# Performance work log

Measured on AMD Instinct MI355X. Metric: run time of the kernel, lower is better.

Reference implementation:

```python
import jax, jax.numpy as jnp
import numpy as np

B, N, DIM = 1, 100_000, 512
HEADS, DIM_HEAD, M = 8, 64, 64


def setup_inputs() -> dict:
    key = jax.random.key(0)
    ks = jax.random.split(key, 9)
    s = 0.04  # ~ kaiming-ish scale for dim=512
    return {
        "x": jax.random.normal(ks[0], (B, N, DIM), dtype=jnp.float32),
        "temperature": jnp.full((1, HEADS, 1, 1), 0.5, dtype=jnp.float32),
        "w_slice": jax.random.normal(ks[1], (HEADS * M, DIM), dtype=jnp.float32) * s,
        "b_slice": jnp.zeros((HEADS * M,), dtype=jnp.float32),
        "w1": jax.random.normal(ks[2], (DIM_HEAD, DIM), dtype=jnp.float32) * s,
        "b1": jnp.zeros((DIM_HEAD,), dtype=jnp.float32),
        "wq": jax.random.normal(ks[3], (DIM_HEAD, DIM_HEAD), dtype=jnp.float32) * 0.125,
        "wk": jax.random.normal(ks[4], (DIM_HEAD, DIM_HEAD), dtype=jnp.float32) * 0.125,
        "wv": jax.random.normal(ks[5], (DIM_HEAD, DIM_HEAD), dtype=jnp.float32) * 0.125,
        "w3": jax.random.normal(ks[6], (DIM_HEAD, DIM_HEAD), dtype=jnp.float32) * 0.125,
        "b3": jnp.zeros((DIM_HEAD,), dtype=jnp.float32),
    }


def reference(x, temperature, w_slice, b_slice, w1, b1, wq, wk, wv, w3, b3):
    b, n, c = x.shape
    # slice logits: (B,N,H*M) -> (B,H,N,M)
    logits = jnp.einsum("bnc,ec->bne", x, w_slice) + b_slice
    logits = logits.reshape(b, n, HEADS, M).transpose(0, 2, 1, 3)
    temp = jnp.clip(temperature, 0.1, 5.0)
    w = jax.nn.softmax(logits / temp, axis=-1)          # (B,H,N,M)
    d = w.sum(axis=2)                                    # (B,H,M)
    # N -> M aggregation (w^T @ x per head)
    s_raw = jnp.einsum("bhnm,bnc->bhmc", w, x)          # (B,H,M,C)
    s = jnp.einsum("bhmc,dc->bhmd", s_raw / (d[..., None] + 1e-5), w1) + b1  # (B,H,M,dh)
    q = jnp.einsum("bhmd,ed->bhme", s, wq)
    k = jnp.einsum("bhmd,ed->bhme", s, wk)
    v = jnp.einsum("bhmd,ed->bhme", s, wv)
    scale = 1.0 / jnp.sqrt(jnp.asarray(DIM_HEAD, dtype=s.dtype))
    attn = jax.nn.softmax(jnp.einsum("bhme,bhle->bhml", q, k) * scale, axis=-1)
    s_att = jnp.einsum("bhml,bhle->bhme", attn, v)      # (B,H,M,dh)
    s_out = jnp.einsum("bhme,de->bhmd", s_att, w3) + b3
    # deslice: w @ s_out -> (B,H,N,dh) -> (B,N,H*dh)
    x_out = jnp.einsum("bhnm,bhmd->bhnd", w, s_out)
    return x_out.transpose(0, 2, 1, 3).reshape(b, n, HEADS * DIM_HEAD)
```

## Files before the change

kernel.cpp:

```cpp
#include <hip/hip_runtime.h>

typedef _Float16 f16;
typedef _Float16 f16x8 __attribute__((ext_vector_type(8)));
typedef _Float16 f16x4 __attribute__((ext_vector_type(4)));
typedef float    f32x4 __attribute__((ext_vector_type(4)));

#define N_TOK   100000
#define NPAD    100032
#define NT1     1563
#define CDIM    512
#define KSTEPS  (NPAD/32)
#define K2SPL   128

#define O_WT     ((size_t)0)
#define SZ_WT    ((size_t)512*NPAD*2)
#define O_YT     (O_WT + SZ_WT)
#define SZ_YT    ((size_t)64*NPAD*2)
#define O_WFR    (O_YT + SZ_YT)
#define SZ_WFR   ((size_t)16*4*9*64*8*2)
#define O_SPP    (O_WFR + SZ_WFR)
#define SZ_SPP   ((size_t)K2SPL*32768*4)
#define O_DPP    (O_SPP + SZ_SPP)
#define SZ_DPP   ((size_t)K2SPL*512*4)
#define O_SPRE   (O_DPP + SZ_DPP)
#define SZ_SPRE  ((size_t)32768*4)
#define O_DSTD   (O_SPRE + SZ_SPRE)
#define SZ_DSTD  ((size_t)512*4)
#define O_SOUT   (O_DSTD + SZ_DSTD)
#define SZ_SOUT  ((size_t)8*64*64*2)

__global__ void k0_pack(const float* __restrict__ wsf, const float* __restrict__ w1f,
                        f16* __restrict__ wfr) {
    int c = blockIdx.x * 256 + threadIdx.x;
    int lane = c & 63, g = c >> 6;
    int u  = g % 9,  r = g / 9;
    int we = r & 3,  kg = r >> 2;
    int col = lane & 15, quad = lane >> 4;
    int k = kg * 32 + quad * 8;
    const float* src;
    if (u < 8) src = wsf + (size_t)(we*128 + u*16 + col) * CDIM + k;
    else       src = w1f + (size_t)(we*16  + col) * CDIM + k;
    float4 a = *(const float4*)(src);
    float4 b = *(const float4*)(src + 4);
    f16x8 h;
    h[0]=(f16)a.x; h[1]=(f16)a.y; h[2]=(f16)a.z; h[3]=(f16)a.w;
    h[4]=(f16)b.x; h[5]=(f16)b.y; h[6]=(f16)b.z; h[7]=(f16)b.w;
    *(f16x8*)(wfr + (size_t)c * 8) = h;
}

#define XROW 40
#define TPITCH 72
__launch_bounds__(256, 3)
__global__ void k1_slice(const float* __restrict__ x, const float* __restrict__ temperature,
                         const f16* __restrict__ wfr, const float* __restrict__ bsl,
                         f16* __restrict__ wT, f16* __restrict__ yT) {
    __shared__ f16 smem[256 * TPITCH];
    f16* lX = smem;
    f16* lT = smem;

    const int tid  = threadIdx.x;
    const int wave = tid >> 6;
    const int lane = tid & 63;
    const int quad = lane >> 4;
    const int col  = lane & 15;

    const int b = blockIdx.x;
    int nt, hg;
    if (b < 3120) { nt = (b >> 4) * 8 + (b & 7); hg = (b >> 3) & 1; }
    else          { nt = 1560 + ((b - 3120) >> 1); hg = (b - 3120) & 1; }
    const int hgrp = hg;
    const int n0   = nt * 64;
    const int h    = hgrp * 4 + wave;

    const int srow = tid >> 2, sch = tid & 3;
    int snr = n0 + srow; if (snr > N_TOK - 1) snr = N_TOK - 1;
    const float* sbase = x + (size_t)snr * CDIM + sch * 8;

    {
        float4 a = *(const float4*)(sbase);
        float4 bb = *(const float4*)(sbase + 4);
        f16x8 hh;
        hh[0]=(f16)a.x; hh[1]=(f16)a.y; hh[2]=(f16)a.z; hh[3]=(f16)a.w;
        hh[4]=(f16)bb.x; hh[5]=(f16)bb.y; hh[6]=(f16)bb.z; hh[7]=(f16)bb.w;
        *(f16x8*)(&lX[srow * XROW + sch * 8]) = hh;
    }

    f32x4 acc[4][5];
    #pragma unroll
    for (int nf = 0; nf < 4; ++nf)
        #pragma unroll
        for (int u = 0; u < 5; ++u) acc[nf][u] = f32x4{0.f,0.f,0.f,0.f};

    __syncthreads();

    #pragma unroll 2
    for (int kg = 0; kg < 16; ++kg) {
        const f16* wb = wfr + ((size_t)(kg*4 + (h >> 1)) * 9 + (size_t)(h & 1) * 4) * 512
                            + (size_t)lane * 8;
        f16x8 bf[4];
        #pragma unroll
        for (int j = 0; j < 4; ++j) bf[j] = *(const f16x8*)(wb + j * 512);
        f16x8 bfy;
        if (hgrp == 0)
            bfy = *(const f16x8*)(wfr + ((size_t)(kg*4 + wave) * 9 + 8) * 512 + (size_t)lane * 8);

        float4 xa, xb;
        if (kg < 15) {
            xa = *(const float4*)(sbase + (kg + 1) * 32);
            xb = *(const float4*)(sbase + (kg + 1) * 32 + 4);
        }

        const f16* xbuf = lX + (kg & 1) * (64 * XROW);
        f16x8 af[4];
        #pragma unroll
        for (int nf = 0; nf < 4; ++nf)
            af[nf] = *(const f16x8*)(xbuf + (nf*16 + col) * XROW + quad * 8);

        #pragma unroll
        for (int nf = 0; nf < 4; ++nf)
            #pragma unroll
            for (int j = 0; j < 4; ++j)
                acc[nf][j] = __builtin_amdgcn_mfma_f32_16x16x32_f16(af[nf], bf[j], acc[nf][j], 0, 0, 0);
        if (hgrp == 0) {
            #pragma unroll
            for (int nf = 0; nf < 4; ++nf)
                acc[nf][4] = __builtin_amdgcn_mfma_f32_16x16x32_f16(af[nf], bfy, acc[nf][4], 0, 0, 0);
        }

        if (kg < 15) {
            f16x8 hh;
            hh[0]=(f16)xa.x; hh[1]=(f16)xa.y; hh[2]=(f16)xa.z; hh[3]=(f16)xa.w;
            hh[4]=(f16)xb.x; hh[5]=(f16)xb.y; hh[6]=(f16)xb.z; hh[7]=(f16)xb.w;
            *(f16x8*)(&lX[((kg + 1) & 1) * (64 * XROW) + srow * XROW + sch * 8]) = hh;
        }
        __syncthreads();
    }

    #pragma unroll
    for (int j = 0; j < 4; ++j) {
        float bb = bsl[h*64 + j*16 + col];
        #pragma unroll
        for (int nf = 0; nf < 4; ++nf)
            #pragma unroll
            for (int r = 0; r < 4; ++r) acc[nf][j][r] += bb;
    }
    float tv = temperature[h];
    tv = fminf(fmaxf(tv, 0.1f), 5.0f);
    const float invt = 1.0f / tv;

    #pragma unroll
    for (int nf = 0; nf < 4; ++nf) {
        const int nloc = nf*16 + quad*4;
        float mx[4];
        #pragma unroll
        for (int r = 0; r < 4; ++r) {
            float m01 = fmaxf(acc[nf][0][r], acc[nf][1][r]);
            float m23 = fmaxf(acc[nf][2][r], acc[nf][3][r]);
            mx[r] = fmaxf(m01, m23);
        }
        #pragma unroll
        for (int d = 1; d < 16; d <<= 1)
            #pragma unroll
            for (int r = 0; r < 4; ++r) mx[r] = fmaxf(mx[r], __shfl_xor(mx[r], d));
        float sm[4] = {0.f, 0.f, 0.f, 0.f};
        #pragma unroll
        for (int j = 0; j < 4; ++j)
            #pragma unroll
            for (int r = 0; r < 4; ++r) {
                float ev = __expf((acc[nf][j][r] - mx[r]) * invt);
                acc[nf][j][r] = ev;
                sm[r] += ev;
            }
        #pragma unroll
        for (int d = 1; d < 16; d <<= 1)
            #pragma unroll
            for (int r = 0; r < 4; ++r) sm[r] += __shfl_xor(sm[r], d);
        #pragma unroll
        for (int r = 0; r < 4; ++r) sm[r] = 1.0f / sm[r];
        #pragma unroll
        for (int j = 0; j < 4; ++j) {
            f16x4 pk;
            #pragma unroll
            for (int r = 0; r < 4; ++r) {
                int n = n0 + nloc + r;
                float wv = (n < N_TOK) ? acc[nf][j][r] * sm[r] : 0.0f;
                pk[r] = (f16)wv;
            }
            int e_loc = wave*64 + j*16 + col;
            *(f16x4*)(lT + (size_t)e_loc*TPITCH + nloc) = pk;
        }
        if (hgrp == 0) {
            f16x4 pk;
            #pragma unroll
            for (int r = 0; r < 4; ++r) {
                int n = n0 + nloc + r;
                pk[r] = (n < N_TOK) ? (f16)acc[nf][4][r] : (f16)0.f;
            }
            *(f16x4*)(yT + (size_t)(wave*16 + col) * NPAD + n0 + nloc) = pk;
        }
    }
    __syncthreads();

    #pragma unroll
    for (int i = 0; i < 8; ++i) {
        int id = tid + i*256;
        int e = id >> 3, p = id & 7;
        f16x8 v = *(const f16x8*)(lT + (size_t)e*TPITCH + p*8);
        *(f16x8*)(wT + (size_t)(hgrp*256 + e)*NPAD + n0 + p*8) = v;
    }
}

#define K2_LOAD(AF, BF, kss)                                                         \
    {   int nb_ = (kss)*32 + quad*8;                                                 \
        _Pragma("unroll")                                                            \
        for (int v = 0; v < 4; ++v)                                                  \
            BF[v] = *(const f16x8*)(yT + (size_t)(v*16 + col)*NPAD + nb_);           \
        _Pragma("unroll")                                                            \
        for (int u = 0; u < 2; ++u)                                                  \
            AF[u] = *(const f16x8*)(wT + (size_t)(ebase + u*16 + col)*NPAD + nb_);   \
    }
#define K2_MFMA(AF, BF)                                                              \
    {   _Pragma("unroll")                                                            \
        for (int u = 0; u < 2; ++u) {                                                \
            _Pragma("unroll")                                                        \
            for (int v = 0; v < 4; ++v)                                              \
                acc[u][v] = __builtin_amdgcn_mfma_f32_16x16x32_f16(AF[u], BF[v], acc[u][v], 0, 0, 0); \
            float s_ = 0.f;                                                          \
            _Pragma("unroll")                                                        \
            for (int j = 0; j < 8; ++j) s_ += (float)AF[u][j];                       \
            dac[u] += s_;                                                            \
        }                                                                            \
    }
__launch_bounds__(256, 4)
__global__ void k2_spre(const f16* __restrict__ wT, const f16* __restrict__ yT,
                        float* __restrict__ spp, float* __restrict__ dpp) {
    const int tid = threadIdx.x, wave = tid >> 6, lane = tid & 63;
    const int quad = lane >> 4, col = lane & 15;
    const int slot = blockIdx.x >> 2, equad = blockIdx.x & 3;
    const int ebase = equad * 128 + wave * 32;

    const int ks0 = (slot * KSTEPS) >> 7;
    const int ks1 = ((slot + 1) * KSTEPS) >> 7;

    f32x4 acc[2][4];
    float dac[2];
    #pragma unroll
    for (int u = 0; u < 2; ++u) {
        dac[u] = 0.f;
        #pragma unroll
        for (int v = 0; v < 4; ++v) acc[u][v] = f32x4{0.f,0.f,0.f,0.f};
    }

    f16x8 afA[2], bfA[4], afB[2], bfB[4];
    K2_LOAD(afA, bfA, ks0)
    int ks = ks0;
    for (; ks + 2 <= ks1; ks += 2) {
        K2_LOAD(afB, bfB, ks + 1)
        K2_MFMA(afA, bfA)
        K2_LOAD(afA, bfA, ks + 2)
        K2_MFMA(afB, bfB)
    }
    if (ks < ks1) K2_MFMA(afA, bfA)

    #pragma unroll
    for (int u = 0; u < 2; ++u) {
        dac[u] += __shfl_xor(dac[u], 16);
        dac[u] += __shfl_xor(dac[u], 32);
    }
    if (quad == 0) {
        #pragma unroll
        for (int u = 0; u < 2; ++u)
            dpp[slot*512 + ebase + u*16 + col] = dac[u];
    }
    float* dst = spp + (size_t)slot * 32768 + (size_t)equad * 8192;
    #pragma unroll
    for (int u = 0; u < 2; ++u)
        #pragma unroll
        for (int v = 0; v < 4; ++v)
            *(f32x4*)(dst + (size_t)((wave*2 + u)*4 + v)*256 + (size_t)lane*4) = acc[u][v];
}

__global__ void k2r_reduce(const float* __restrict__ spp, const float* __restrict__ dpp,
                           float* __restrict__ spre, float* __restrict__ dstd) {
    int i = blockIdx.x*256 + threadIdx.x;
    float s = 0.f;
    for (int p = 0; p < K2SPL; ++p) s += spp[(size_t)p*32768 + i];
    int r = i & 3, L = (i >> 2) & 63, v = (i >> 8) & 3, g = (i >> 10) & 7, eq = (i >> 13) & 3;
    int e = eq*128 + (g >> 1)*32 + (g & 1)*16 + (L >> 4)*4 + r;
    int d = v*16 + (L & 15);
    spre[e*64 + d] = s;
    if (i < 512) {
        float tt = 0.f;
        for (int p = 0; p < K2SPL; ++p) tt += dpp[p*512 + i];
        dstd[i] = tt;
    }
}

__global__ void k3_attn(const float* __restrict__ spre, const float* __restrict__ dstd,
                        const float* __restrict__ b1, const float* __restrict__ wq,
                        const float* __restrict__ wk, const float* __restrict__ wv,
                        const float* __restrict__ w3, const float* __restrict__ b3,
                        f16* __restrict__ sout) {
    __shared__ float wa[64][65], wb[64][65], wc[64][65];
    __shared__ float ss[64][65], kk[64][65], vv[64][65];
    __shared__ float qq[16][65], sc[16][65];
    const int h = blockIdx.x >> 2, ms = blockIdx.x & 3, tid = threadIdx.x;

    for (int i = tid; i < 4096; i += 256) {
        int r = i >> 6, c = i & 63;
        wa[r][c] = wq[i];
        wb[r][c] = wk[i];
        wc[r][c] = wv[i];
        ss[r][c] = spre[h*4096 + i] / (dstd[h*64 + r] + 1e-5f) + b1[c];
    }
    __syncthreads();

    #pragma unroll
    for (int it = 0; it < 16; ++it) {
        int m = it*4 + (tid >> 6), e = tid & 63;
        float ak = 0.f, av = 0.f;
        #pragma unroll 8
        for (int d = 0; d < 64; ++d) {
            float sv = ss[m][d];
            ak += sv * wb[e][d];
            av += sv * wc[e][d];
        }
        kk[m][e] = ak; vv[m][e] = av;
    }
    #pragma unroll
    for (int it = 0; it < 4; ++it) {
        int ml = it*4 + (tid >> 6), e = tid & 63;
        float aq = 0.f;
        #pragma unroll 8
        for (int d = 0; d < 64; ++d) aq += ss[ms*16 + ml][d] * wa[e][d];
        qq[ml][e] = aq;
    }
    __syncthreads();

    for (int i = tid; i < 4096; i += 256) wa[i >> 6][i & 63] = w3[i];
    #pragma unroll
    for (int it = 0; it < 4; ++it) {
        int ml = it*4 + (tid >> 6), l = tid & 63;
        float a = 0.f;
        #pragma unroll 8
        for (int e = 0; e < 64; ++e) a += qq[ml][e] * kk[l][e];
        sc[ml][l] = a * 0.125f;
    }
    __syncthreads();

    if (tid < 16) {
        int ml = tid;
        float mx = -1e30f;
        #pragma unroll 8
        for (int l = 0; l < 64; ++l) mx = fmaxf(mx, sc[ml][l]);
        float sm = 0.f;
        #pragma unroll 8
        for (int l = 0; l < 64; ++l) { float ev = __expf(sc[ml][l] - mx); sc[ml][l] = ev; sm += ev; }
        float rs = 1.0f / sm;
        #pragma unroll 8
        for (int l = 0; l < 64; ++l) sc[ml][l] *= rs;
    }
    __syncthreads();

    #pragma unroll
    for (int it = 0; it < 4; ++it) {
        int ml = it*4 + (tid >> 6), e = tid & 63;
        float a = 0.f;
        #pragma unroll 8
        for (int l = 0; l < 64; ++l) a += sc[ml][l] * vv[l][e];
        qq[ml][e] = a;
    }
    __syncthreads();

    #pragma unroll
    for (int it = 0; it < 4; ++it) {
        int d = it*16 + (tid >> 4), ml = tid & 15;
        float a = b3[d];
        #pragma unroll 8
        for (int e = 0; e < 64; ++e) a += qq[ml][e] * wa[d][e];
        sout[(h*64 + d)*64 + ms*16 + ml] = (f16)a;
    }
}

#define K4PITCH 36
__launch_bounds__(256, 4)
__global__ void k4_deslice(const f16* __restrict__ wT, const f16* __restrict__ sout,
                           float* __restrict__ out) {
    __shared__ __align__(16) char lmem[512 * K4PITCH * 2];
    f16*   ldsW = (f16*)lmem;
    float* ldsO = (float*)lmem;

    const int tid = threadIdx.x, wave = tid >> 6, lane = tid & 63;
    const int quad = lane >> 4, col = lane & 15;

    const int bid = blockIdx.x;
    const int xcd = bid & 7, idx = bid >> 3;
    const int q = KSTEPS >> 3, r = KSTEPS & 7;
    const int swz = (xcd < r ? xcd*(q+1) : r*(q+1) + (xcd - r)*q) + idx;
    const int n0 = swz * 32;

    #pragma unroll
    for (int i = 0; i < 8; ++i) {
        int id = tid + i*256;
        int e = id >> 2, p = id & 3;
        f16x8 v = *(const f16x8*)(wT + (size_t)e*NPAD + n0 + p*8);
        *(f16x8*)(ldsW + (size_t)e*K4PITCH + p*8) = v;
    }
    __syncthreads();

    f32x4 acc[2][2][4];
    #pragma unroll
    for (int hh = 0; hh < 2; ++hh)
        #pragma unroll
        for (int t = 0; t < 2; ++t)
            #pragma unroll
            for (int v = 0; v < 4; ++v) acc[hh][t][v] = f32x4{0.f,0.f,0.f,0.f};

    #pragma unroll
    for (int hh = 0; hh < 2; ++hh) {
        int h = wave*2 + hh;
        #pragma unroll
        for (int ks = 0; ks < 2; ++ks) {
            f16x8 af[2], bf[4];
            #pragma unroll
            for (int t = 0; t < 2; ++t) {
                f16x8 a;
                #pragma unroll
                for (int j = 0; j < 8; ++j)
                    a[j] = ldsW[(size_t)(h*64 + ks*32 + quad*8 + j)*K4PITCH + t*16 + col];
                af[t] = a;
            }
            #pragma unroll
            for (int v = 0; v < 4; ++v)
                bf[v] = *(const f16x8*)(sout + (size_t)(h*64 + v*16 + col)*64 + ks*32 + quad*8);
            #pragma unroll
            for (int t = 0; t < 2; ++t)
                #pragma unroll
                for (int v = 0; v < 4; ++v)
                    acc[hh][t][v] = __builtin_amdgcn_mfma_f32_16x16x32_f16(af[t], bf[v], acc[hh][t][v], 0, 0, 0);
        }
    }

    #pragma unroll
    for (int p = 0; p < 2; ++p) {
        __syncthreads();
        #pragma unroll
        for (int hh = 0; hh < 2; ++hh) {
            int h = wave*2 + hh;
            #pragma unroll
            for (int v = 0; v < 4; ++v)
                #pragma unroll
                for (int r2 = 0; r2 < 4; ++r2)
                    ldsO[(size_t)(quad*4 + r2)*516 + h*64 + v*16 + col] = acc[hh][p][v][r2];
        }
        __syncthreads();
        #pragma unroll
        for (int it = 0; it < 8; ++it) {
            int id = tid + it*256;
            int row = id >> 7, ch = id & 127;
            int n = n0 + p*16 + row;
            if (n < N_TOK) {
                float4 v4 = *(const float4*)(ldsO + (size_t)row*516 + ch*4);
                *(float4*)(out + (size_t)n*512 + ch*4) = v4;
            }
        }
    }
}

extern "C" void kernel_launch(void* const* d_in, const int* in_sizes, int n_in,
                              void* d_out, int out_size, void* d_ws, size_t ws_size,
                              hipStream_t stream) {
    const float* x           = (const float*)d_in[0];
    const float* temperature = (const float*)d_in[1];
    const float* w_slice     = (const float*)d_in[2];
    const float* b_slice     = (const float*)d_in[3];
    const float* w1          = (const float*)d_in[4];
    const float* b1          = (const float*)d_in[5];
    const float* wq          = (const float*)d_in[6];
    const float* wk          = (const float*)d_in[7];
    const float* wv          = (const float*)d_in[8];
    const float* w3          = (const float*)d_in[9];
    const float* b3          = (const float*)d_in[10];
    float* out = (float*)d_out;
    char*  ws  = (char*)d_ws;

    f16*   wT    = (f16*)(ws + O_WT);
    f16*   yT    = (f16*)(ws + O_YT);
    f16*   wfr   = (f16*)(ws + O_WFR);
    float* spp   = (float*)(ws + O_SPP);
    float* dpp   = (float*)(ws + O_DPP);
    float* spre  = (float*)(ws + O_SPRE);
    float* dstd  = (float*)(ws + O_DSTD);
    f16*   sout  = (f16*)(ws + O_SOUT);

    k0_pack<<<144, 256, 0, stream>>>(w_slice, w1, wfr);
    k1_slice<<<NT1*2, 256, 0, stream>>>(x, temperature, wfr, b_slice, wT, yT);
    k2_spre<<<K2SPL*4, 256, 0, stream>>>(wT, yT, spp, dpp);
    k2r_reduce<<<128, 256, 0, stream>>>(spp, dpp, spre, dstd);
    k3_attn<<<32, 256, 0, stream>>>(spre, dstd, b1, wq, wk, wv, w3, b3, sout);
    k4_deslice<<<KSTEPS, 256, 0, stream>>>(wT, sout, out);
}
```

Before: 563.0 us.

## Split slice kernel work across more blocks with 2 heads per block

```diff
diff --git a/kernel.cpp b/kernel.cpp
--- a/kernel.cpp
+++ b/kernel.cpp
@@ -50,27 +50,27 @@
 
 #define XROW 40
 #define TPITCH 72
-__launch_bounds__(256, 3)
+__launch_bounds__(256, 4)
 __global__ void k1_slice(const float* __restrict__ x, const float* __restrict__ temperature,
                          const f16* __restrict__ wfr, const float* __restrict__ bsl,
                          f16* __restrict__ wT, f16* __restrict__ yT) {
-    __shared__ f16 smem[256 * TPITCH];
+    __shared__ f16 smem[128 * TPITCH];
     f16* lX = smem;
     f16* lT = smem;
 
     const int tid  = threadIdx.x;
-    const int wave = tid >> 6;
+    const int w    = tid >> 6;
     const int lane = tid & 63;
     const int quad = lane >> 4;
     const int col  = lane & 15;
 
     const int b = blockIdx.x;
     int nt, hg;
-    if (b < 3120) { nt = (b >> 4) * 8 + (b & 7); hg = (b >> 3) & 1; }
-    else          { nt = 1560 + ((b - 3120) >> 1); hg = (b - 3120) & 1; }
-    const int hgrp = hg;
-    const int n0   = nt * 64;
-    const int h    = hgrp * 4 + wave;
+    if (b < 6240) { nt = (b >> 5) * 8 + (b & 7); hg = (b >> 3) & 3; }
+    else          { int t = b - 6240; nt = 1560 + (t >> 2); hg = t & 3; }
+    const int n0 = nt * 64;
+    const int hd = hg * 2 + (w & 1);
+    const int nh = w >> 1;
 
     const int srow = tid >> 2, sch = tid & 3;
     int snr = n0 + srow; if (snr > N_TOK - 1) snr = N_TOK - 1;
@@ -85,24 +85,32 @@
         *(f16x8*)(&lX[srow * XROW + sch * 8]) = hh;
     }
 
-    f32x4 acc[4][5];
-    #pragma unroll
-    for (int nf = 0; nf < 4; ++nf)
-        #pragma unroll
-        for (int u = 0; u < 5; ++u) acc[nf][u] = f32x4{0.f,0.f,0.f,0.f};
+    f32x4 accS[2][4];
+    f32x4 accY[2][2];
+    #pragma unroll
+    for (int nf = 0; nf < 2; ++nf) {
+        #pragma unroll
+        for (int j = 0; j < 4; ++j) accS[nf][j] = f32x4{0.f,0.f,0.f,0.f};
+        #pragma unroll
+        for (int jy = 0; jy < 2; ++jy) accY[nf][jy] = f32x4{0.f,0.f,0.f,0.f};
+    }
 
     __syncthreads();
 
     #pragma unroll 2
     for (int kg = 0; kg < 16; ++kg) {
-        const f16* wb = wfr + ((size_t)(kg*4 + (h >> 1)) * 9 + (size_t)(h & 1) * 4) * 512
+        const f16* wb = wfr + ((size_t)(kg*4 + (hd >> 1)) * 9 + (size_t)(hd & 1) * 4) * 512
                             + (size_t)lane * 8;
         f16x8 bf[4];
         #pragma unroll
         for (int j = 0; j < 4; ++j) bf[j] = *(const f16x8*)(wb + j * 512);
-        f16x8 bfy;
-        if (hgrp == 0)
-            bfy = *(const f16x8*)(wfr + ((size_t)(kg*4 + wave) * 9 + 8) * 512 + (size_t)lane * 8);
+        f16x8 bfy[2];
+        if (hg == 0) {
+            #pragma unroll
+            for (int jy = 0; jy < 2; ++jy)
+                bfy[jy] = *(const f16x8*)(wfr + ((size_t)(kg*4 + ((w & 1)*2 + jy)) * 9 + 8) * 512
+                                               + (size_t)lane * 8);
+        }
 
         float4 xa, xb;
         if (kg < 15) {
@@ -111,20 +119,22 @@
         }
 
         const f16* xbuf = lX + (kg & 1) * (64 * XROW);
-        f16x8 af[4];
-        #pragma unroll
-        for (int nf = 0; nf < 4; ++nf)
-            af[nf] = *(const f16x8*)(xbuf + (nf*16 + col) * XROW + quad * 8);
-
-        #pragma unroll
-        for (int nf = 0; nf < 4; ++nf)
+        f16x8 af[2];
+        #pragma unroll
+        for (int nf = 0; nf < 2; ++nf)
+            af[nf] = *(const f16x8*)(xbuf + (nh*32 + nf*16 + col) * XROW + quad * 8);
+
+        #pragma unroll
+        for (int nf = 0; nf < 2; ++nf)
             #pragma unroll
             for (int j = 0; j < 4; ++j)
-                acc[nf][j] = __builtin_amdgcn_mfma_f32_16x16x32_f16(af[nf], bf[j], acc[nf][j], 0, 0, 0);
-        if (hgrp == 0) {
-            #pragma unroll
-            for (int nf = 0; nf < 4; ++nf)
-                acc[nf][4] = __builtin_amdgcn_mfma_f32_16x16x32_f16(af[nf], bfy, acc[nf][4], 0, 0, 0);
+                accS[nf][j] = __builtin_amdgcn_mfma_f32_16x16x32_f16(af[nf], bf[j], accS[nf][j], 0, 0, 0);
+        if (hg == 0) {
+            #pragma unroll
+            for (int nf = 0; nf < 2; ++nf)
+                #pragma unroll
+                for (int jy = 0; jy < 2; ++jy)
+                    accY[nf][jy] = __builtin_amdgcn_mfma_f32_16x16x32_f16(af[nf], bfy[jy], accY[nf][jy], 0, 0, 0);
         }
 
         if (kg < 15) {
@@ -138,24 +148,24 @@
 
     #pragma unroll
     for (int j = 0; j < 4; ++j) {
-        float bb = bsl[h*64 + j*16 + col];
-        #pragma unroll
-        for (int nf = 0; nf < 4; ++nf)
-            #pragma unroll
-            for (int r = 0; r < 4; ++r) acc[nf][j][r] += bb;
-    }
-    float tv = temperature[h];
+        float bb = bsl[hd*64 + j*16 + col];
+        #pragma unroll
+        for (int nf = 0; nf < 2; ++nf)
+            #pragma unroll
+            for (int r = 0; r < 4; ++r) accS[nf][j][r] += bb;
+    }
+    float tv = temperature[hd];
     tv = fminf(fmaxf(tv, 0.1f), 5.0f);
     const float invt = 1.0f / tv;
 
     #pragma unroll
-    for (int nf = 0; nf < 4; ++nf) {
-        const int nloc = nf*16 + quad*4;
+    for (int nf = 0; nf < 2; ++nf) {
+        const int nloc = nh*32 + nf*16 + quad*4;
         float mx[4];
         #pragma unroll
         for (int r = 0; r < 4; ++r) {
-            float m01 = fmaxf(acc[nf][0][r], acc[nf][1][r]);
-            float m23 = fmaxf(acc[nf][2][r], acc[nf][3][r]);
+            float m01 = fmaxf(accS[nf][0][r], accS[nf][1][r]);
+            float m23 = fmaxf(accS[nf][2][r], accS[nf][3][r]);
             mx[r] = fmaxf(m01, m23);
         }
         #pragma unroll
@@ -167,8 +177,8 @@
         for (int j = 0; j < 4; ++j)
             #pragma unroll
             for (int r = 0; r < 4; ++r) {
-                float ev = __expf((acc[nf][j][r] - mx[r]) * invt);
-                acc[nf][j][r] = ev;
+                float ev = __expf((accS[nf][j][r] - mx[r]) * invt);
+                accS[nf][j][r] = ev;
                 sm[r] += ev;
             }
         #pragma unroll
@@ -183,30 +193,34 @@
             #pragma unroll
             for (int r = 0; r < 4; ++r) {
                 int n = n0 + nloc + r;
-                float wv = (n < N_TOK) ? acc[nf][j][r] * sm[r] : 0.0f;
+                float wv = (n < N_TOK) ? accS[nf][j][r] * sm[r] : 0.0f;
                 pk[r] = (f16)wv;
             }
-            int e_loc = wave*64 + j*16 + col;
+            int e_loc = (w & 1)*64 + j*16 + col;
             *(f16x4*)(lT + (size_t)e_loc*TPITCH + nloc) = pk;
         }
-        if (hgrp == 0) {
-            f16x4 pk;
-            #pragma unroll
-            for (int r = 0; r < 4; ++r) {
-                int n = n0 + nloc + r;
-                pk[r] = (n < N_TOK) ? (f16)acc[nf][4][r] : (f16)0.f;
+        if (hg == 0) {
+            #pragma unroll
+            for (int jy = 0; jy < 2; ++jy) {
+                f16x4 pk;
+                #pragma unroll
+                for (int r = 0; r < 4; ++r) {
+                    int n = n0 + nloc + r;
+                    pk[r] = (n < N_TOK) ? (f16)accY[nf][jy][r] : (f16)0.f;
+                }
+                int d = ((w & 1)*2 + jy)*16 + col;
+                *(f16x4*)(yT + (size_t)d * NPAD + n0 + nloc) = pk;
             }
-            *(f16x4*)(yT + (size_t)(wave*16 + col) * NPAD + n0 + nloc) = pk;
-        }
-    }
-    __syncthreads();
-
-    #pragma unroll
-    for (int i = 0; i < 8; ++i) {
+        }
+    }
+    __syncthreads();
+
+    #pragma unroll
+    for (int i = 0; i < 4; ++i) {
         int id = tid + i*256;
         int e = id >> 3, p = id & 7;
         f16x8 v = *(const f16x8*)(lT + (size_t)e*TPITCH + p*8);
-        *(f16x8*)(wT + (size_t)(hgrp*256 + e)*NPAD + n0 + p*8) = v;
+        *(f16x8*)(wT + (size_t)(hg*128 + e)*NPAD + n0 + p*8) = v;
     }
 }
 
@@ -303,8 +317,8 @@
                         f16* __restrict__ sout) {
     __shared__ float wa[64][65], wb[64][65], wc[64][65];
     __shared__ float ss[64][65], kk[64][65], vv[64][65];
-    __shared__ float qq[16][65], sc[16][65];
-    const int h = blockIdx.x >> 2, ms = blockIdx.x & 3, tid = threadIdx.x;
+    __shared__ float qq[8][65], sc[8][65];
+    const int h = blockIdx.x >> 3, ms = blockIdx.x & 7, tid = threadIdx.x;
 
     for (int i = tid; i < 4096; i += 256) {
         int r = i >> 6, c = i & 63;
@@ -328,18 +342,18 @@
         kk[m][e] = ak; vv[m][e] = av;
     }
     #pragma unroll
-    for (int it = 0; it < 4; ++it) {
+    for (int it = 0; it < 2; ++it) {
         int ml = it*4 + (tid >> 6), e = tid & 63;
         float aq = 0.f;
         #pragma unroll 8
-        for (int d = 0; d < 64; ++d) aq += ss[ms*16 + ml][d] * wa[e][d];
+        for (int d = 0; d < 64; ++d) aq += ss[ms*8 + ml][d] * wa[e][d];
         qq[ml][e] = aq;
     }
     __syncthreads();
 
     for (int i = tid; i < 4096; i += 256) wa[i >> 6][i & 63] = w3[i];
     #pragma unroll
-    for (int it = 0; it < 4; ++it) {
+    for (int it = 0; it < 2; ++it) {
         int ml = it*4 + (tid >> 6), l = tid & 63;
         float a = 0.f;
         #pragma unroll 8
@@ -348,7 +362,7 @@
     }
     __syncthreads();
 
-    if (tid < 16) {
+    if (tid < 8) {
         int ml = tid;
         float mx = -1e30f;
         #pragma unroll 8
@@ -363,7 +377,7 @@
     __syncthreads();
 
     #pragma unroll
-    for (int it = 0; it < 4; ++it) {
+    for (int it = 0; it < 2; ++it) {
         int ml = it*4 + (tid >> 6), e = tid & 63;
         float a = 0.f;
         #pragma unroll 8
@@ -373,12 +387,12 @@
     __syncthreads();
 
     #pragma unroll
-    for (int it = 0; it < 4; ++it) {
-        int d = it*16 + (tid >> 4), ml = tid & 15;
+    for (int it = 0; it < 2; ++it) {
+        int d = it*32 + (tid >> 3), ml = tid & 7;
         float a = b3[d];
         #pragma unroll 8
         for (int e = 0; e < 64; ++e) a += qq[ml][e] * wa[d][e];
-        sout[(h*64 + d)*64 + ms*16 + ml] = (f16)a;
+        sout[(h*64 + d)*64 + ms*8 + ml] = (f16)a;
     }
 }
 
@@ -494,9 +508,9 @@
     f16*   sout  = (f16*)(ws + O_SOUT);
 
     k0_pack<<<144, 256, 0, stream>>>(w_slice, w1, wfr);
-    k1_slice<<<NT1*2, 256, 0, stream>>>(x, temperature, wfr, b_slice, wT, yT);
+    k1_slice<<<NT1*4, 256, 0, stream>>>(x, temperature, wfr, b_slice, wT, yT);
     k2_spre<<<K2SPL*4, 256, 0, stream>>>(wT, yT, spp, dpp);
     k2r_reduce<<<128, 256, 0, stream>>>(spp, dpp, spre, dstd);
-    k3_attn<<<32, 256, 0, stream>>>(spre, dstd, b1, wq, wk, wv, w3, b3, sout);
+    k3_attn<<<64, 256, 0, stream>>>(spre, dstd, b1, wq, wk, wv, w3, b3, sout);
     k4_deslice<<<KSTEPS, 256, 0, stream>>>(wT, sout, out);
 }
```

New measurement: 589.3 us. 1.05x slower.

## Stage x in 128-column chunks in k1 and split k3 across more blocks

Applied to the files above, without the earlier changes.

```diff
diff --git a/kernel.cpp b/kernel.cpp
--- a/kernel.cpp
+++ b/kernel.cpp
@@ -48,7 +48,7 @@
     *(f16x8*)(wfr + (size_t)c * 8) = h;
 }
 
-#define XROW 40
+#define XR128 136
 #define TPITCH 72
 __launch_bounds__(256, 3)
 __global__ void k1_slice(const float* __restrict__ x, const float* __restrict__ temperature,
@@ -63,26 +63,22 @@
     const int lane = tid & 63;
     const int quad = lane >> 4;
     const int col  = lane & 15;
-
-    const int b = blockIdx.x;
-    int nt, hg;
-    if (b < 3120) { nt = (b >> 4) * 8 + (b & 7); hg = (b >> 3) & 1; }
-    else          { nt = 1560 + ((b - 3120) >> 1); hg = (b - 3120) & 1; }
-    const int hgrp = hg;
-    const int n0   = nt * 64;
+    const int hgrp = blockIdx.x & 1;
+    const int n0   = (blockIdx.x >> 1) * 64;
     const int h    = hgrp * 4 + wave;
 
     const int srow = tid >> 2, sch = tid & 3;
     int snr = n0 + srow; if (snr > N_TOK - 1) snr = N_TOK - 1;
     const float* sbase = x + (size_t)snr * CDIM + sch * 8;
 
-    {
-        float4 a = *(const float4*)(sbase);
-        float4 bb = *(const float4*)(sbase + 4);
+    #pragma unroll
+    for (int c = 0; c < 4; ++c) {
+        float4 a  = *(const float4*)(sbase + c * 32);
+        float4 bb = *(const float4*)(sbase + c * 32 + 4);
         f16x8 hh;
-        hh[0]=(f16)a.x; hh[1]=(f16)a.y; hh[2]=(f16)a.z; hh[3]=(f16)a.w;
+        hh[0]=(f16)a.x;  hh[1]=(f16)a.y;  hh[2]=(f16)a.z;  hh[3]=(f16)a.w;
         hh[4]=(f16)bb.x; hh[5]=(f16)bb.y; hh[6]=(f16)bb.z; hh[7]=(f16)bb.w;
-        *(f16x8*)(&lX[srow * XROW + sch * 8]) = hh;
+        *(f16x8*)(&lX[srow * XR128 + c * 32 + sch * 8]) = hh;
     }
 
     f32x4 acc[4][5];
@@ -93,45 +89,55 @@
 
     __syncthreads();
 
-    #pragma unroll 2
-    for (int kg = 0; kg < 16; ++kg) {
-        const f16* wb = wfr + ((size_t)(kg*4 + (h >> 1)) * 9 + (size_t)(h & 1) * 4) * 512
-                            + (size_t)lane * 8;
-        f16x8 bf[4];
-        #pragma unroll
-        for (int j = 0; j < 4; ++j) bf[j] = *(const f16x8*)(wb + j * 512);
-        f16x8 bfy;
-        if (hgrp == 0)
-            bfy = *(const f16x8*)(wfr + ((size_t)(kg*4 + wave) * 9 + 8) * 512 + (size_t)lane * 8);
-
-        float4 xa, xb;
-        if (kg < 15) {
-            xa = *(const float4*)(sbase + (kg + 1) * 32);
-            xb = *(const float4*)(sbase + (kg + 1) * 32 + 4);
-        }
-
-        const f16* xbuf = lX + (kg & 1) * (64 * XROW);
-        f16x8 af[4];
-        #pragma unroll
-        for (int nf = 0; nf < 4; ++nf)
-            af[nf] = *(const f16x8*)(xbuf + (nf*16 + col) * XROW + quad * 8);
-
-        #pragma unroll
-        for (int nf = 0; nf < 4; ++nf)
-            #pragma unroll
-            for (int j = 0; j < 4; ++j)
-                acc[nf][j] = __builtin_amdgcn_mfma_f32_16x16x32_f16(af[nf], bf[j], acc[nf][j], 0, 0, 0);
-        if (hgrp == 0) {
+    for (int kgo = 0; kgo < 4; ++kgo) {
+        float4 nxa[4], nxb[4];
+        if (kgo < 3) {
+            #pragma unroll
+            for (int c = 0; c < 4; ++c) {
+                nxa[c] = *(const float4*)(sbase + (kgo + 1) * 128 + c * 32);
+                nxb[c] = *(const float4*)(sbase + (kgo + 1) * 128 + c * 32 + 4);
+            }
+        }
+
+        const f16* xbuf = lX + (kgo & 1) * (64 * XR128);
+        #pragma unroll
+        for (int kk = 0; kk < 4; ++kk) {
+            const int kg = kgo * 4 + kk;
+            const f16* wb = wfr + ((size_t)(kg*4 + (h >> 1)) * 9 + (size_t)(h & 1) * 4) * 512
+                                + (size_t)lane * 8;
+            f16x8 bf[4];
+            #pragma unroll
+            for (int j = 0; j < 4; ++j) bf[j] = *(const f16x8*)(wb + j * 512);
+            f16x8 bfy;
+            if (hgrp == 0)
+                bfy = *(const f16x8*)(wfr + ((size_t)(kg*4 + wave) * 9 + 8) * 512 + (size_t)lane * 8);
+
+            f16x8 af[4];
             #pragma unroll
             for (int nf = 0; nf < 4; ++nf)
-                acc[nf][4] = __builtin_amdgcn_mfma_f32_16x16x32_f16(af[nf], bfy, acc[nf][4], 0, 0, 0);
-        }
-
-        if (kg < 15) {
-            f16x8 hh;
-            hh[0]=(f16)xa.x; hh[1]=(f16)xa.y; hh[2]=(f16)xa.z; hh[3]=(f16)xa.w;
-            hh[4]=(f16)xb.x; hh[5]=(f16)xb.y; hh[6]=(f16)xb.z; hh[7]=(f16)xb.w;
-            *(f16x8*)(&lX[((kg + 1) & 1) * (64 * XROW) + srow * XROW + sch * 8]) = hh;
+                af[nf] = *(const f16x8*)(xbuf + (nf*16 + col) * XR128 + kk * 32 + quad * 8);
+
+            #pragma unroll
+            for (int nf = 0; nf < 4; ++nf)
+                #pragma unroll
+                for (int j = 0; j < 4; ++j)
+                    acc[nf][j] = __builtin_amdgcn_mfma_f32_16x16x32_f16(af[nf], bf[j], acc[nf][j], 0, 0, 0);
+            if (hgrp == 0) {
+                #pragma unroll
+                for (int nf = 0; nf < 4; ++nf)
+                    acc[nf][4] = __builtin_amdgcn_mfma_f32_16x16x32_f16(af[nf], bfy, acc[nf][4], 0, 0, 0);
+            }
+        }
+
+        if (kgo < 3) {
+            f16* dstb = lX + ((kgo + 1) & 1) * (64 * XR128);
+            #pragma unroll
+            for (int c = 0; c < 4; ++c) {
+                f16x8 hh;
+                hh[0]=(f16)nxa[c].x; hh[1]=(f16)nxa[c].y; hh[2]=(f16)nxa[c].z; hh[3]=(f16)nxa[c].w;
+                hh[4]=(f16)nxb[c].x; hh[5]=(f16)nxb[c].y; hh[6]=(f16)nxb[c].z; hh[7]=(f16)nxb[c].w;
+                *(f16x8*)(&dstb[srow * XR128 + c * 32 + sch * 8]) = hh;
+            }
         }
         __syncthreads();
     }
@@ -303,8 +309,8 @@
                         f16* __restrict__ sout) {
     __shared__ float wa[64][65], wb[64][65], wc[64][65];
     __shared__ float ss[64][65], kk[64][65], vv[64][65];
-    __shared__ float qq[16][65], sc[16][65];
-    const int h = blockIdx.x >> 2, ms = blockIdx.x & 3, tid = threadIdx.x;
+    __shared__ float qq[8][65], sc[8][65];
+    const int h = blockIdx.x >> 3, ms = blockIdx.x & 7, tid = threadIdx.x;
 
     for (int i = tid; i < 4096; i += 256) {
         int r = i >> 6, c = i & 63;
@@ -328,18 +334,18 @@
         kk[m][e] = ak; vv[m][e] = av;
     }
     #pragma unroll
-    for (int it = 0; it < 4; ++it) {
+    for (int it = 0; it < 2; ++it) {
         int ml = it*4 + (tid >> 6), e = tid & 63;
         float aq = 0.f;
         #pragma unroll 8
-        for (int d = 0; d < 64; ++d) aq += ss[ms*16 + ml][d] * wa[e][d];
+        for (int d = 0; d < 64; ++d) aq += ss[ms*8 + ml][d] * wa[e][d];
         qq[ml][e] = aq;
     }
     __syncthreads();
 
     for (int i = tid; i < 4096; i += 256) wa[i >> 6][i & 63] = w3[i];
     #pragma unroll
-    for (int it = 0; it < 4; ++it) {
+    for (int it = 0; it < 2; ++it) {
         int ml = it*4 + (tid >> 6), l = tid & 63;
         float a = 0.f;
         #pragma unroll 8
@@ -348,7 +354,7 @@
     }
     __syncthreads();
 
-    if (tid < 16) {
+    if (tid < 8) {
         int ml = tid;
         float mx = -1e30f;
         #pragma unroll 8
@@ -363,7 +369,7 @@
     __syncthreads();
 
     #pragma unroll
-    for (int it = 0; it < 4; ++it) {
+    for (int it = 0; it < 2; ++it) {
         int ml = it*4 + (tid >> 6), e = tid & 63;
         float a = 0.f;
         #pragma unroll 8
@@ -373,12 +379,12 @@
     __syncthreads();
 
     #pragma unroll
-    for (int it = 0; it < 4; ++it) {
-        int d = it*16 + (tid >> 4), ml = tid & 15;
+    for (int it = 0; it < 2; ++it) {
+        int d = it*32 + (tid >> 3), ml = tid & 7;
         float a = b3[d];
         #pragma unroll 8
         for (int e = 0; e < 64; ++e) a += qq[ml][e] * wa[d][e];
-        sout[(h*64 + d)*64 + ms*16 + ml] = (f16)a;
+        sout[(h*64 + d)*64 + ms*8 + ml] = (f16)a;
     }
 }
 
@@ -497,6 +503,6 @@
     k1_slice<<<NT1*2, 256, 0, stream>>>(x, temperature, wfr, b_slice, wT, yT);
     k2_spre<<<K2SPL*4, 256, 0, stream>>>(wT, yT, spp, dpp);
     k2r_reduce<<<128, 256, 0, stream>>>(spp, dpp, spre, dstd);
-    k3_attn<<<32, 256, 0, stream>>>(spre, dstd, b1, wq, wk, wv, w3, b3, sout);
+    k3_attn<<<64, 256, 0, stream>>>(spre, dstd, b1, wq, wk, wv, w3, b3, sout);
     k4_deslice<<<KSTEPS, 256, 0, stream>>>(wT, sout, out);
 }
```

Result: slower. 587.6 us (+4.4%).

## Store slice weights in MFMA-fragment-major layout and split attention across more blocks

Applied to the files above, without the earlier changes.

```diff
diff --git a/kernel.cpp b/kernel.cpp
--- a/kernel.cpp
+++ b/kernel.cpp
@@ -53,22 +53,19 @@
 __launch_bounds__(256, 3)
 __global__ void k1_slice(const float* __restrict__ x, const float* __restrict__ temperature,
                          const f16* __restrict__ wfr, const float* __restrict__ bsl,
-                         f16* __restrict__ wT, f16* __restrict__ yT) {
-    __shared__ f16 smem[256 * TPITCH];
+                         f16* __restrict__ wTf, f16* __restrict__ yTf) {
+    __shared__ f16 smem[320 * TPITCH];
     f16* lX = smem;
     f16* lT = smem;
+    f16* lY = smem + 256 * TPITCH;
 
     const int tid  = threadIdx.x;
     const int wave = tid >> 6;
     const int lane = tid & 63;
     const int quad = lane >> 4;
     const int col  = lane & 15;
-
-    const int b = blockIdx.x;
-    int nt, hg;
-    if (b < 3120) { nt = (b >> 4) * 8 + (b & 7); hg = (b >> 3) & 1; }
-    else          { nt = 1560 + ((b - 3120) >> 1); hg = (b - 3120) & 1; }
-    const int hgrp = hg;
+    const int hgrp = blockIdx.x & 1;
+    const int nt   = blockIdx.x >> 1;
     const int n0   = nt * 64;
     const int h    = hgrp * 4 + wave;
 
@@ -196,28 +193,42 @@
                 int n = n0 + nloc + r;
                 pk[r] = (n < N_TOK) ? (f16)acc[nf][4][r] : (f16)0.f;
             }
-            *(f16x4*)(yT + (size_t)(wave*16 + col) * NPAD + n0 + nloc) = pk;
+            *(f16x4*)(lY + (size_t)(wave*16 + col)*TPITCH + nloc) = pk;
         }
     }
     __syncthreads();
 
     #pragma unroll
     for (int i = 0; i < 8; ++i) {
-        int id = tid + i*256;
-        int e = id >> 3, p = id & 7;
-        f16x8 v = *(const f16x8*)(lT + (size_t)e*TPITCH + p*8);
-        *(f16x8*)(wT + (size_t)(hgrp*256 + e)*NPAD + n0 + p*8) = v;
+        int gid = tid + i*256;
+        int laneL = gid & 63, chunk = gid >> 6;
+        int ks_loc = chunk >> 4, floc = chunk & 15;
+        f16x8 v = *(const f16x8*)(lT + (size_t)(floc*16 + (laneL & 15))*TPITCH
+                                     + ks_loc*32 + (laneL >> 4)*8);
+        *(f16x8*)(wTf + ((size_t)((nt*2 + ks_loc)*32 + hgrp*16 + floc))*512
+                       + (size_t)laneL*8) = v;
+    }
+    if (hgrp == 0) {
+        #pragma unroll
+        for (int i = 0; i < 2; ++i) {
+            int gid = tid + i*256;
+            int laneL = gid & 63, chunk = gid >> 6;
+            int ks_loc = chunk >> 2, v4 = chunk & 3;
+            f16x8 vv = *(const f16x8*)(lY + (size_t)(v4*16 + (laneL & 15))*TPITCH
+                                          + ks_loc*32 + (laneL >> 4)*8);
+            *(f16x8*)(yTf + ((size_t)((nt*2 + ks_loc)*4 + v4))*512
+                           + (size_t)laneL*8) = vv;
+        }
     }
 }
 
 #define K2_LOAD(AF, BF, kss)                                                         \
-    {   int nb_ = (kss)*32 + quad*8;                                                 \
-        _Pragma("unroll")                                                            \
+    {   _Pragma("unroll")                                                            \
         for (int v = 0; v < 4; ++v)                                                  \
-            BF[v] = *(const f16x8*)(yT + (size_t)(v*16 + col)*NPAD + nb_);           \
+            BF[v] = *(const f16x8*)(yTf + ((size_t)((kss)*4 + v))*512 + (size_t)lane*8); \
         _Pragma("unroll")                                                            \
         for (int u = 0; u < 2; ++u)                                                  \
-            AF[u] = *(const f16x8*)(wT + (size_t)(ebase + u*16 + col)*NPAD + nb_);   \
+            AF[u] = *(const f16x8*)(wTf + ((size_t)((kss)*32 + fbase + u))*512 + (size_t)lane*8); \
     }
 #define K2_MFMA(AF, BF)                                                              \
     {   _Pragma("unroll")                                                            \
@@ -232,12 +243,13 @@
         }                                                                            \
     }
 __launch_bounds__(256, 4)
-__global__ void k2_spre(const f16* __restrict__ wT, const f16* __restrict__ yT,
+__global__ void k2_spre(const f16* __restrict__ wTf, const f16* __restrict__ yTf,
                         float* __restrict__ spp, float* __restrict__ dpp) {
     const int tid = threadIdx.x, wave = tid >> 6, lane = tid & 63;
     const int quad = lane >> 4, col = lane & 15;
     const int slot = blockIdx.x >> 2, equad = blockIdx.x & 3;
     const int ebase = equad * 128 + wave * 32;
+    const int fbase = equad * 8 + wave * 2;
 
     const int ks0 = (slot * KSTEPS) >> 7;
     const int ks1 = ((slot + 1) * KSTEPS) >> 7;
@@ -303,8 +315,8 @@
                         f16* __restrict__ sout) {
     __shared__ float wa[64][65], wb[64][65], wc[64][65];
     __shared__ float ss[64][65], kk[64][65], vv[64][65];
-    __shared__ float qq[16][65], sc[16][65];
-    const int h = blockIdx.x >> 2, ms = blockIdx.x & 3, tid = threadIdx.x;
+    __shared__ float qq[8][65], sc[8][65];
+    const int h = blockIdx.x >> 3, ms = blockIdx.x & 7, tid = threadIdx.x;
 
     for (int i = tid; i < 4096; i += 256) {
         int r = i >> 6, c = i & 63;
@@ -328,18 +340,18 @@
         kk[m][e] = ak; vv[m][e] = av;
     }
     #pragma unroll
-    for (int it = 0; it < 4; ++it) {
+    for (int it = 0; it < 2; ++it) {
         int ml = it*4 + (tid >> 6), e = tid & 63;
         float aq = 0.f;
         #pragma unroll 8
-        for (int d = 0; d < 64; ++d) aq += ss[ms*16 + ml][d] * wa[e][d];
+        for (int d = 0; d < 64; ++d) aq += ss[ms*8 + ml][d] * wa[e][d];
         qq[ml][e] = aq;
     }
     __syncthreads();
 
     for (int i = tid; i < 4096; i += 256) wa[i >> 6][i & 63] = w3[i];
     #pragma unroll
-    for (int it = 0; it < 4; ++it) {
+    for (int it = 0; it < 2; ++it) {
         int ml = it*4 + (tid >> 6), l = tid & 63;
         float a = 0.f;
         #pragma unroll 8
@@ -348,7 +360,7 @@
     }
     __syncthreads();
 
-    if (tid < 16) {
+    if (tid < 8) {
         int ml = tid;
         float mx = -1e30f;
         #pragma unroll 8
@@ -363,7 +375,7 @@
     __syncthreads();
 
     #pragma unroll
-    for (int it = 0; it < 4; ++it) {
+    for (int it = 0; it < 2; ++it) {
         int ml = it*4 + (tid >> 6), e = tid & 63;
         float a = 0.f;
         #pragma unroll 8
@@ -373,20 +385,19 @@
     __syncthreads();
 
     #pragma unroll
-    for (int it = 0; it < 4; ++it) {
-        int d = it*16 + (tid >> 4), ml = tid & 15;
+    for (int it = 0; it < 2; ++it) {
+        int d = it*32 + (tid >> 3), ml = tid & 7;
         float a = b3[d];
         #pragma unroll 8
         for (int e = 0; e < 64; ++e) a += qq[ml][e] * wa[d][e];
-        sout[(h*64 + d)*64 + ms*16 + ml] = (f16)a;
-    }
-}
-
-#define K4PITCH 36
+        sout[(h*64 + d)*64 + ms*8 + ml] = (f16)a;
+    }
+}
+
 __launch_bounds__(256, 4)
-__global__ void k4_deslice(const f16* __restrict__ wT, const f16* __restrict__ sout,
+__global__ void k4_deslice(const f16* __restrict__ wTf, const f16* __restrict__ sout,
                            float* __restrict__ out) {
-    __shared__ __align__(16) char lmem[512 * K4PITCH * 2];
+    __shared__ __align__(16) char lmem[36864];
     f16*   ldsW = (f16*)lmem;
     float* ldsO = (float*)lmem;
 
@@ -399,12 +410,11 @@
     const int swz = (xcd < r ? xcd*(q+1) : r*(q+1) + (xcd - r)*q) + idx;
     const int n0 = swz * 32;
 
+    const f16* srcW = wTf + (size_t)swz * 16384;
     #pragma unroll
     for (int i = 0; i < 8; ++i) {
         int id = tid + i*256;
-        int e = id >> 2, p = id & 3;
-        f16x8 v = *(const f16x8*)(wT + (size_t)e*NPAD + n0 + p*8);
-        *(f16x8*)(ldsW + (size_t)e*K4PITCH + p*8) = v;
+        *(f16x8*)(ldsW + (size_t)id*8) = *(const f16x8*)(srcW + (size_t)id*8);
     }
     __syncthreads();
 
@@ -424,10 +434,12 @@
             f16x8 af[2], bf[4];
             #pragma unroll
             for (int t = 0; t < 2; ++t) {
+                const int fb = (h*4 + ks*2 + (quad >> 1))*512
+                             + (t*2 + (col >> 3))*128 + (quad & 1)*64 + (col & 7);
                 f16x8 a;
                 #pragma unroll
                 for (int j = 0; j < 8; ++j)
-                    a[j] = ldsW[(size_t)(h*64 + ks*32 + quad*8 + j)*K4PITCH + t*16 + col];
+                    a[j] = ldsW[fb + j*8];
                 af[t] = a;
             }
             #pragma unroll
@@ -484,8 +496,8 @@
     float* out = (float*)d_out;
     char*  ws  = (char*)d_ws;
 
-    f16*   wT    = (f16*)(ws + O_WT);
-    f16*   yT    = (f16*)(ws + O_YT);
+    f16*   wTf   = (f16*)(ws + O_WT);
+    f16*   yTf   = (f16*)(ws + O_YT);
     f16*   wfr   = (f16*)(ws + O_WFR);
     float* spp   = (float*)(ws + O_SPP);
     float* dpp   = (float*)(ws + O_DPP);
@@ -494,9 +506,9 @@
     f16*   sout  = (f16*)(ws + O_SOUT);
 
     k0_pack<<<144, 256, 0, stream>>>(w_slice, w1, wfr);
-    k1_slice<<<NT1*2, 256, 0, stream>>>(x, temperature, wfr, b_slice, wT, yT);
-    k2_spre<<<K2SPL*4, 256, 0, stream>>>(wT, yT, spp, dpp);
+    k1_slice<<<NT1*2, 256, 0, stream>>>(x, temperature, wfr, b_slice, wTf, yTf);
+    k2_spre<<<K2SPL*4, 256, 0, stream>>>(wTf, yTf, spp, dpp);
     k2r_reduce<<<128, 256, 0, stream>>>(spp, dpp, spre, dstd);
-    k3_attn<<<32, 256, 0, stream>>>(spre, dstd, b1, wq, wk, wv, w3, b3, sout);
-    k4_deslice<<<KSTEPS, 256, 0, stream>>>(wT, sout, out);
-}
+    k3_attn<<<64, 256, 0, stream>>>(spre, dstd, b1, wq, wk, wv, w3, b3, sout);
+    k4_deslice<<<KSTEPS, 256, 0, stream>>>(wTf, sout, out);
+}
```

Result: faster. 546.0 us (-3.0%).
